# Kernel tuning notes

Measured on AMD Instinct MI355X. Metric: run time of the kernel, lower is better.

The kernel has to match this reference:

```python
import jax, jax.numpy as jnp
import numpy as np

DIM = 64
N_ITER = 2
NUM_USR = 50000
NUM_ENT = 200000
NUM_REL = 32
N_NEIGHBOR = 16
BATCH = 4096


def setup_inputs() -> dict:
    key = jax.random.key(0)
    ks = jax.random.split(key, 12)
    u = jax.random.randint(ks[0], (BATCH,), 0, NUM_USR)
    v = jax.random.randint(ks[1], (BATCH,), 0, NUM_ENT)
    adj = jax.random.randint(ks[2], (NUM_ENT, N_NEIGHBOR), 0, NUM_ENT)
    rel_adj = jax.random.randint(ks[3], (NUM_ENT, N_NEIGHBOR), 0, NUM_REL + 1)
    usr_emb = jax.random.normal(ks[4], (NUM_USR, DIM), dtype=jnp.float32)
    ent_emb = jax.random.normal(ks[5], (NUM_ENT, DIM), dtype=jnp.float32)
    rel_emb = jax.random.normal(ks[6], (NUM_REL + 1, DIM), dtype=jnp.float32)
    # per-hop aggregator Linear(dim, dim) weights (applied as x @ W + b)
    scale = 1.0 / np.sqrt(DIM)
    W0 = jax.random.uniform(ks[7], (DIM, DIM), jnp.float32, -scale, scale)
    b0 = jax.random.uniform(ks[8], (DIM,), jnp.float32, -scale, scale)
    W1 = jax.random.uniform(ks[9], (DIM, DIM), jnp.float32, -scale, scale)
    b1 = jax.random.uniform(ks[10], (DIM,), jnp.float32, -scale, scale)
    return {"u": u, "v": v, "adj": adj, "rel_adj": rel_adj,
            "usr_emb": usr_emb, "ent_emb": ent_emb, "rel_emb": rel_emb,
            "W0": W0, "b0": b0, "W1": W1, "b1": b1}


def reference(u, v, adj, rel_adj, usr_emb, ent_emb, rel_emb, W0, b0, W1, b1):
    B = u.shape[0]
    user = usr_emb[u]  # [B, D]

    # multi-hop neighbor index expansion
    entities = [v[:, None]]            # hop h: [B, n^h]
    relations = []
    for h in range(N_ITER):
        ne = adj[entities[h]].reshape(B, -1)      # [B, n^(h+1)]
        nr = rel_adj[entities[h]].reshape(B, -1)
        entities.append(ne)
        relations.append(nr)

    ent_vecs = [ent_emb[e] for e in entities]     # [B, n^h, D]
    rel_vecs = [rel_emb[r] for r in relations]

    Ws, bs = [W0, W1], [b0, b1]
    for i in range(N_ITER):
        act = jnp.tanh if i == N_ITER - 1 else jax.nn.sigmoid
        nxt = []
        for hop in range(N_ITER - i):
            sv = ent_vecs[hop]                                        # [B, m, D]
            nv = ent_vecs[hop + 1].reshape(B, -1, N_NEIGHBOR, DIM)    # [B, m, n, D]
            nr = rel_vecs[hop].reshape(B, -1, N_NEIGHBOR, DIM)        # [B, m, n, D]
            # user-relation attention over neighbors
            scores = jnp.einsum('bd,bmnd->bmn', user, nr)
            attn = jax.nn.softmax(scores, axis=-1)
            agg = jnp.einsum('bmn,bmnd->bmd', attn, nv)
            out = act((sv + agg) @ Ws[i] + bs[i])
            nxt.append(out)
        ent_vecs = nxt

    item = ent_vecs[0].reshape(B, DIM)
    return jax.nn.sigmoid(jnp.sum(user * item, axis=1))
```

## Files before the change

kernel.cpp:

```cpp
#include <hip/hip_runtime.h>
#include <hip/hip_fp16.h>

#define DIMN 64
#define NNB 16
#define NREL 33
#define WPB 4
#define XSTR 68
#define WFRAG_BYTES 16384

typedef float        floatx4 __attribute__((ext_vector_type(4)));
typedef short        shortx8 __attribute__((ext_vector_type(8)));
typedef unsigned int uintx2  __attribute__((ext_vector_type(2)));

__device__ __forceinline__ float bcastf(float x, int lane) {
    return __int_as_float(__builtin_amdgcn_readlane(__float_as_int(x), lane));
}

__global__ void prep_kernel(const float* __restrict__ W0, unsigned short* __restrict__ wsp,
                            const float* __restrict__ ent, __half* __restrict__ ent16,
                            long n4)
{
    const long tid = (long)blockIdx.x * blockDim.x + threadIdx.x;
    if (tid < 512) {
        const int l = (int)tid & 63;
        const int t = ((int)tid >> 6) & 3;
        const int ks = (int)tid >> 8;
        const int k0 = ks * 32 + (l >> 4) * 8;
        const int n  = t * 16 + (l & 15);
        const unsigned base = ((unsigned)(ks * 4 + t) * 64 + l) * 8;
        #pragma unroll
        for (int j = 0; j < 8; ++j) {
            const float x = W0[(k0 + j) * DIMN + n];
            const unsigned u  = __float_as_uint(x);
            const unsigned uh = u & 0xFFFF0000u;
            const float lf = x - __uint_as_float(uh);
            wsp[base + j]        = (unsigned short)(u >> 16);
            wsp[4096 + base + j] = (unsigned short)(__float_as_uint(lf) >> 16);
        }
    }
    if (ent16) {
        const long stride = (long)gridDim.x * blockDim.x;
        for (long i = tid; i < n4; i += stride) {
            const float4 x = ((const float4*)ent)[i];
            __half2 a = __floats2half2_rn(x.x, x.y);
            __half2 b = __floats2half2_rn(x.z, x.w);
            ((__half2*)ent16)[2 * i]     = a;
            ((__half2*)ent16)[2 * i + 1] = b;
        }
    }
}

__device__ __forceinline__ floatx4 cvt4(uintx2 raw) {
    union { unsigned int u; __half2 h; } a, b;
    a.u = raw.x; b.u = raw.y;
    const float2 f01 = __half22float2(a.h);
    const float2 f23 = __half22float2(b.h);
    return (floatx4){f01.x, f01.y, f23.x, f23.y};
}

template<bool F16>
__global__ __launch_bounds__(64 * WPB, 4)
void kgs_kernel(const int* __restrict__ u, const int* __restrict__ v,
                const int* __restrict__ adj, const int* __restrict__ rel_adj,
                const float* __restrict__ usr_emb, const float* __restrict__ ent_emb,
                const __half* __restrict__ ent16,
                const float* __restrict__ rel_emb,
                const float* __restrict__ W0, const float* __restrict__ b0,
                const float* __restrict__ W1, const float* __restrict__ b1,
                const unsigned short* __restrict__ wsp,
                float* __restrict__ out, int B)
{
    const int tid  = threadIdx.x;
    const int wid  = tid >> 6;
    const int d    = tid & 63;
    const int n16  = d & 15;
    const int quad = d >> 4;
    int b = blockIdx.x * WPB + wid;
    if (b >= B) b = B - 1;

    __shared__ __align__(16) float user_sh[WPB][DIMN];
    __shared__ float ur_sh[WPB][NREL + 3];
    __shared__ __align__(16) float sv_sh[WPB][NNB * XSTR];
    __shared__ __align__(16) float gbuf[WPB][NNB * XSTR];

    const int uu = u[b];
    const int vv = v[b];

    const float user_d = usr_emb[(size_t)uu * DIMN + d];
    const int e1n = adj[vv * NNB + n16];
    const int r1n = rel_adj[vv * NNB + n16];
    float sv0;
    if constexpr (F16) sv0 = __half2float(ent16[(size_t)vv * DIMN + d]);
    else               sv0 = ent_emb[(size_t)vv * DIMN + d];
    user_sh[wid][d] = user_d;

    floatx4 svv[4];
    #pragma unroll
    for (int q = 0; q < 4; ++q) {
        const int em = __shfl(e1n, 4 * q + quad);
        if constexpr (F16)
            svv[q] = cvt4(*(const uintx2*)(ent16 + (size_t)em * DIMN + 4 * n16));
        else
            svv[q] = *(const floatx4*)(ent_emb + (size_t)em * DIMN + 4 * n16);
    }

    int e2n_r[NNB], r2n_r[NNB];
    #pragma unroll
    for (int m = 0; m < NNB; ++m) {
        const int em = __builtin_amdgcn_readlane(e1n, m);
        e2n_r[m] = adj[em * NNB + n16];
        r2n_r[m] = rel_adj[em * NNB + n16];
    }

    if (d < NREL) {
        const float* re = rel_emb + d * DIMN;
        float acc = 0.f;
        #pragma unroll
        for (int k = 0; k < DIMN; k += 4) {
            const float4 uk = *(const float4*)(&user_sh[wid][k]);
            const float4 rk = *(const float4*)(re + k);
            acc = fmaf(uk.x, rk.x, acc);
            acc = fmaf(uk.y, rk.y, acc);
            acc = fmaf(uk.z, rk.z, acc);
            acc = fmaf(uk.w, rk.w, acc);
        }
        ur_sh[wid][d] = acc;
    }

    #pragma unroll
    for (int q = 0; q < 4; ++q)
        *(floatx4*)(&sv_sh[wid][(4 * q + quad) * XSTR + 4 * n16]) = svv[q];

    float attn[NNB];
    #pragma unroll
    for (int m = 0; m < NNB; ++m) {
        const float e = __expf(ur_sh[wid][r2n_r[m]]);
        float s = e;
        s += __shfl_xor(s, 1);
        s += __shfl_xor(s, 2);
        s += __shfl_xor(s, 4);
        s += __shfl_xor(s, 8);
        attn[m] = e * __builtin_amdgcn_rcpf(s);
    }

    #pragma unroll
    for (int m = 0; m < NNB; ++m) {
        floatx4 acc4 = (floatx4){0.f, 0.f, 0.f, 0.f};
        #pragma unroll
        for (int q = 0; q < 4; ++q) {
            const int src = 4 * q + quad;
            const int en  = __shfl(e2n_r[m], src);
            floatx4 g;
            if constexpr (F16)
                g = cvt4(*(const uintx2*)(ent16 + (size_t)en * DIMN + 4 * n16));
            else
                g = *(const floatx4*)(ent_emb + (size_t)en * DIMN + 4 * n16);
            const float aw = __shfl(attn[m], src);
            acc4[0] = fmaf(aw, g[0], acc4[0]);
            acc4[1] = fmaf(aw, g[1], acc4[1]);
            acc4[2] = fmaf(aw, g[2], acc4[2]);
            acc4[3] = fmaf(aw, g[3], acc4[3]);
        }
        #pragma unroll
        for (int c = 0; c < 4; ++c) {
            acc4[c] += __shfl_xor(acc4[c], 16);
            acc4[c] += __shfl_xor(acc4[c], 32);
        }
        if (d < 16)
            *(floatx4*)(&gbuf[wid][m * XSTR + 4 * d]) = acc4;
    }

    shortx8 Ahi[2], Alo[2];
    #pragma unroll
    for (int ks = 0; ks < 2; ++ks) {
        const int off = (d & 15) * XSTR + quad * 8 + ks * 32;
        const floatx4 sa = *(const floatx4*)(&sv_sh[wid][off]);
        const floatx4 sb = *(const floatx4*)(&sv_sh[wid][off + 4]);
        const floatx4 ga = *(const floatx4*)(&gbuf[wid][off]);
        const floatx4 gb = *(const floatx4*)(&gbuf[wid][off + 4]);
        unsigned uh[8], ul[8];
        #pragma unroll
        for (int j = 0; j < 8; ++j) {
            const float x = (j < 4) ? (sa[j] + ga[j]) : (sb[j - 4] + gb[j - 4]);
            const unsigned ub = __float_as_uint(x);
            uh[j] = ub & 0xFFFF0000u;
            ul[j] = __float_as_uint(x - __uint_as_float(uh[j]));
        }
        union { int i[4]; shortx8 s; } ch, cl;
        #pragma unroll
        for (int p = 0; p < 4; ++p) {
            ch.i[p] = (int)(uh[2 * p + 1] | (uh[2 * p] >> 16));
            cl.i[p] = (int)((ul[2 * p + 1] & 0xFFFF0000u) | (ul[2 * p] >> 16));
        }
        Ahi[ks] = ch.s;
        Alo[ks] = cl.s;
    }

    const shortx8* wf = (const shortx8*)wsp;
    floatx4 acc[4];
    #pragma unroll
    for (int t = 0; t < 4; ++t) acc[t] = (floatx4){0.f, 0.f, 0.f, 0.f};
    #pragma unroll
    for (int t = 0; t < 4; ++t) {
        #pragma unroll
        for (int ks = 0; ks < 2; ++ks) {
            const int f = ks * 4 + t;
            const shortx8 bhi = wf[f * 64 + d];
            const shortx8 blo = wf[512 + f * 64 + d];
            acc[t] = __builtin_amdgcn_mfma_f32_16x16x32_bf16(Ahi[ks], bhi, acc[t], 0, 0, 0);
            acc[t] = __builtin_amdgcn_mfma_f32_16x16x32_bf16(Ahi[ks], blo, acc[t], 0, 0, 0);
            acc[t] = __builtin_amdgcn_mfma_f32_16x16x32_bf16(Alo[ks], bhi, acc[t], 0, 0, 0);
        }
    }

    #pragma unroll
    for (int t = 0; t < 4; ++t) {
        const float bv = b0[t * 16 + n16];
        #pragma unroll
        for (int reg = 0; reg < 4; ++reg) {
            const float o = acc[t][reg] + bv;
            const int m = quad * 4 + reg;
            gbuf[wid][m * XSTR + t * 16 + n16] = 1.f / (1.f + __expf(-o));
        }
    }

    const float e0 = __expf(ur_sh[wid][r1n]);
    float sum0 = e0;
    sum0 += __shfl_xor(sum0, 1);
    sum0 += __shfl_xor(sum0, 2);
    sum0 += __shfl_xor(sum0, 4);
    sum0 += __shfl_xor(sum0, 8);
    const float attn0 = e0 * __builtin_amdgcn_rcpf(sum0);

    float agg0 = 0.f, agg1 = 0.f;
    #pragma unroll
    for (int n = 0; n < NNB; ++n) {
        const float an = bcastf(attn0, n);
        agg0 = fmaf(an, sv_sh[wid][n * XSTR + d], agg0);
        agg1 = fmaf(an, gbuf[wid][n * XSTR + d], agg1);
    }

    const float x0 = sv0 + agg0;
    float a0 = 0.f, a1 = 0.f, a2 = 0.f, a3 = 0.f;
    for (int k = 0; k < DIMN; k += 4) {
        const float* wr = W0 + k * DIMN;
        a0 = fmaf(bcastf(x0, k + 0), wr[d], a0);
        a1 = fmaf(bcastf(x0, k + 1), wr[DIMN + d], a1);
        a2 = fmaf(bcastf(x0, k + 2), wr[2 * DIMN + d], a2);
        a3 = fmaf(bcastf(x0, k + 3), wr[3 * DIMN + d], a3);
    }
    const float o0 = b0[d] + ((a0 + a1) + (a2 + a3));
    const float h0 = 1.f / (1.f + __expf(-o0));

    const float x1 = h0 + agg1;
    float c0 = 0.f, c1 = 0.f, c2 = 0.f, c3 = 0.f;
    for (int k = 0; k < DIMN; k += 4) {
        const float* wr = W1 + k * DIMN;
        c0 = fmaf(bcastf(x1, k + 0), wr[d], c0);
        c1 = fmaf(bcastf(x1, k + 1), wr[DIMN + d], c1);
        c2 = fmaf(bcastf(x1, k + 2), wr[2 * DIMN + d], c2);
        c3 = fmaf(bcastf(x1, k + 3), wr[3 * DIMN + d], c3);
    }
    const float o1 = b1[d] + ((c0 + c1) + (c2 + c3));
    const float item_d = 1.f - 2.f / (1.f + __expf(2.f * o1));

    float p = user_d * item_d;
    p += __shfl_xor(p, 1);
    p += __shfl_xor(p, 2);
    p += __shfl_xor(p, 4);
    p += __shfl_xor(p, 8);
    p += __shfl_xor(p, 16);
    p += __shfl_xor(p, 32);
    if (d == 0) out[b] = 1.f / (1.f + __expf(-p));
}

extern "C" void kernel_launch(void* const* d_in, const int* in_sizes, int n_in,
                              void* d_out, int out_size, void* d_ws, size_t ws_size,
                              hipStream_t stream) {
    const int*   u       = (const int*)d_in[0];
    const int*   v       = (const int*)d_in[1];
    const int*   adj     = (const int*)d_in[2];
    const int*   rel_adj = (const int*)d_in[3];
    const float* usr_emb = (const float*)d_in[4];
    const float* ent_emb = (const float*)d_in[5];
    const float* rel_emb = (const float*)d_in[6];
    const float* W0      = (const float*)d_in[7];
    const float* b0      = (const float*)d_in[8];
    const float* W1      = (const float*)d_in[9];
    const float* b1      = (const float*)d_in[10];
    float* out = (float*)d_out;
    unsigned short* wsp = (unsigned short*)d_ws;

    const int B = in_sizes[0];
    const long nent = (long)in_sizes[5];
    const size_t need = (size_t)WFRAG_BYTES + (size_t)nent * sizeof(__half);
    const bool use16 = (ws_size >= need) && ((nent & 3) == 0);
    __half* ent16 = use16 ? (__half*)((char*)d_ws + WFRAG_BYTES) : nullptr;

    const long n4 = nent / 4;
    const int conv_blocks = use16 ? 6400 : 2;
    prep_kernel<<<dim3(conv_blocks), dim3(256), 0, stream>>>(W0, wsp, ent_emb, ent16, n4);

    const int grid = (B + WPB - 1) / WPB;
    if (use16)
        kgs_kernel<true><<<dim3(grid), dim3(64 * WPB), 0, stream>>>(
            u, v, adj, rel_adj, usr_emb, ent_emb, ent16, rel_emb, W0, b0, W1, b1,
            wsp, out, B);
    else
        kgs_kernel<false><<<dim3(grid), dim3(64 * WPB), 0, stream>>>(
            u, v, adj, rel_adj, usr_emb, ent_emb, nullptr, rel_emb, W0, b0, W1, b1,
            wsp, out, B);
}
```

Before: 156.4 us.

## Split each batch element across two wavefronts with block-level sync

Each batch element is now handled by two wavefronts instead of one. Each wave gathers half of the hop-2 neighbours, and the hop-1 MFMA linear and the hop-0 scalar linear run concurrently on different waves. Work is coordinated through shared memory and __syncthreads, and the launch-bounds occupancy hint is raised to 8 blocks. The conversion kernel also packs its fp16 stores into one 64-bit write. The goal is to shorten per-element latency and raise parallelism for the latency-bound gathers, at the cost of block barriers and idle waves in the final stage.

```diff
diff --git a/kernel.cpp b/kernel.cpp
--- a/kernel.cpp
+++ b/kernel.cpp
@@ -4,7 +4,7 @@
 #define DIMN 64
 #define NNB 16
 #define NREL 33
-#define WPB 4
+#define EPB 2
 #define XSTR 68
 #define WFRAG_BYTES 16384
 
@@ -42,10 +42,10 @@
         const long stride = (long)gridDim.x * blockDim.x;
         for (long i = tid; i < n4; i += stride) {
             const float4 x = ((const float4*)ent)[i];
-            __half2 a = __floats2half2_rn(x.x, x.y);
-            __half2 b = __floats2half2_rn(x.z, x.w);
-            ((__half2*)ent16)[2 * i]     = a;
-            ((__half2*)ent16)[2 * i + 1] = b;
+            union { __half2 h[2]; uintx2 u; } pk;
+            pk.h[0] = __floats2half2_rn(x.x, x.y);
+            pk.h[1] = __floats2half2_rn(x.z, x.w);
+            ((uintx2*)ent16)[i] = pk.u;
         }
     }
 }
@@ -59,7 +59,7 @@
 }
 
 template<bool F16>
-__global__ __launch_bounds__(64 * WPB, 4)
+__global__ __launch_bounds__(64 * 4, 8)
 void kgs_kernel(const int* __restrict__ u, const int* __restrict__ v,
                 const int* __restrict__ adj, const int* __restrict__ rel_adj,
                 const float* __restrict__ usr_emb, const float* __restrict__ ent_emb,
@@ -75,13 +75,15 @@
     const int d    = tid & 63;
     const int n16  = d & 15;
     const int quad = d >> 4;
-    int b = blockIdx.x * WPB + wid;
+    const int e    = wid >> 1;
+    const int half = wid & 1;
+    int b = blockIdx.x * EPB + e;
     if (b >= B) b = B - 1;
 
-    __shared__ __align__(16) float user_sh[WPB][DIMN];
-    __shared__ float ur_sh[WPB][NREL + 3];
-    __shared__ __align__(16) float sv_sh[WPB][NNB * XSTR];
-    __shared__ __align__(16) float gbuf[WPB][NNB * XSTR];
+    __shared__ __align__(16) float user_sh[EPB][DIMN];
+    __shared__ float ur_sh[EPB][NREL + 3];
+    __shared__ __align__(16) float sv_sh[EPB][NNB * XSTR];
+    __shared__ __align__(16) float gbuf[EPB][NNB * XSTR];
 
     const int uu = u[b];
     const int vv = v[b];
@@ -92,70 +94,75 @@
     float sv0;
     if constexpr (F16) sv0 = __half2float(ent16[(size_t)vv * DIMN + d]);
     else               sv0 = ent_emb[(size_t)vv * DIMN + d];
-    user_sh[wid][d] = user_d;
-
-    floatx4 svv[4];
+    user_sh[e][d] = user_d;
+
     #pragma unroll
-    for (int q = 0; q < 4; ++q) {
+    for (int qq = 0; qq < 2; ++qq) {
+        const int q  = 2 * half + qq;
         const int em = __shfl(e1n, 4 * q + quad);
+        floatx4 sq;
         if constexpr (F16)
-            svv[q] = cvt4(*(const uintx2*)(ent16 + (size_t)em * DIMN + 4 * n16));
+            sq = cvt4(*(const uintx2*)(ent16 + (size_t)em * DIMN + 4 * n16));
         else
-            svv[q] = *(const floatx4*)(ent_emb + (size_t)em * DIMN + 4 * n16);
-    }
-
-    int e2n_r[NNB], r2n_r[NNB];
+            sq = *(const floatx4*)(ent_emb + (size_t)em * DIMN + 4 * n16);
+        *(floatx4*)(&sv_sh[e][(4 * q + quad) * XSTR + 4 * n16]) = sq;
+    }
+
+    int e2n_r[8], r2n_r[8];
     #pragma unroll
-    for (int m = 0; m < NNB; ++m) {
-        const int em = __builtin_amdgcn_readlane(e1n, m);
-        e2n_r[m] = adj[em * NNB + n16];
-        r2n_r[m] = rel_adj[em * NNB + n16];
-    }
-
-    if (d < NREL) {
-        const float* re = rel_emb + d * DIMN;
-        float acc = 0.f;
-        #pragma unroll
-        for (int k = 0; k < DIMN; k += 4) {
-            const float4 uk = *(const float4*)(&user_sh[wid][k]);
-            const float4 rk = *(const float4*)(re + k);
-            acc = fmaf(uk.x, rk.x, acc);
-            acc = fmaf(uk.y, rk.y, acc);
-            acc = fmaf(uk.z, rk.z, acc);
-            acc = fmaf(uk.w, rk.w, acc);
-        }
-        ur_sh[wid][d] = acc;
-    }
-
+    for (int j = 0; j < 8; ++j) {
+        const int em = __builtin_amdgcn_readlane(e1n, 8 * half + j);
+        e2n_r[j] = adj[em * NNB + n16];
+        r2n_r[j] = rel_adj[em * NNB + n16];
+    }
+
+    {
+        const int lim = half ? 16 : 17;
+        if (d < lim) {
+            const int rr = half * 17 + d;
+            const float* re = rel_emb + rr * DIMN;
+            float acc = 0.f;
+            #pragma unroll
+            for (int k = 0; k < DIMN; k += 4) {
+                const float4 uk = *(const float4*)(&user_sh[e][k]);
+                const float4 rk = *(const float4*)(re + k);
+                acc = fmaf(uk.x, rk.x, acc);
+                acc = fmaf(uk.y, rk.y, acc);
+                acc = fmaf(uk.z, rk.z, acc);
+                acc = fmaf(uk.w, rk.w, acc);
+            }
+            ur_sh[e][rr] = acc;
+        }
+    }
+
+    __syncthreads();
+
+    float attn[8];
     #pragma unroll
-    for (int q = 0; q < 4; ++q)
-        *(floatx4*)(&sv_sh[wid][(4 * q + quad) * XSTR + 4 * n16]) = svv[q];
-
-    float attn[NNB];
-    #pragma unroll
-    for (int m = 0; m < NNB; ++m) {
-        const float e = __expf(ur_sh[wid][r2n_r[m]]);
-        float s = e;
+    for (int j = 0; j < 8; ++j) {
+        const float ex = __expf(ur_sh[e][r2n_r[j]]);
+        float s = ex;
         s += __shfl_xor(s, 1);
         s += __shfl_xor(s, 2);
         s += __shfl_xor(s, 4);
         s += __shfl_xor(s, 8);
-        attn[m] = e * __builtin_amdgcn_rcpf(s);
+        attn[j] = ex * __builtin_amdgcn_rcpf(s);
     }
 
     #pragma unroll
-    for (int m = 0; m < NNB; ++m) {
+    for (int j = 0; j < 8; ++j) {
+        const int m = 8 * half + j;
         floatx4 acc4 = (floatx4){0.f, 0.f, 0.f, 0.f};
         #pragma unroll
         for (int q = 0; q < 4; ++q) {
             const int src = 4 * q + quad;
-            const int en  = __shfl(e2n_r[m], src);
+            const int en  = __shfl(e2n_r[j], src);
             floatx4 g;
             if constexpr (F16)
                 g = cvt4(*(const uintx2*)(ent16 + (size_t)en * DIMN + 4 * n16));
             else
                 g = *(const floatx4*)(ent_emb + (size_t)en * DIMN + 4 * n16);
-            const float aw = __shfl(attn[m], src);
+            const float aw = __shfl(attn[j], src);
             acc4[0] = fmaf(aw, g[0], acc4[0]);
             acc4[1] = fmaf(aw, g[1], acc4[1]);
             acc4[2] = fmaf(aw, g[2], acc4[2]);
@@ -167,111 +174,122 @@
             acc4[c] += __shfl_xor(acc4[c], 32);
         }
         if (d < 16)
-            *(floatx4*)(&gbuf[wid][m * XSTR + 4 * d]) = acc4;
-    }
-
-    shortx8 Ahi[2], Alo[2];
-    #pragma unroll
-    for (int ks = 0; ks < 2; ++ks) {
-        const int off = (d & 15) * XSTR + quad * 8 + ks * 32;
-        const floatx4 sa = *(const floatx4*)(&sv_sh[wid][off]);
-        const floatx4 sb = *(const floatx4*)(&sv_sh[wid][off + 4]);
-        const floatx4 ga = *(const floatx4*)(&gbuf[wid][off]);
-        const floatx4 gb = *(const floatx4*)(&gbuf[wid][off + 4]);
-        unsigned uh[8], ul[8];
-        #pragma unroll
-        for (int j = 0; j < 8; ++j) {
-            const float x = (j < 4) ? (sa[j] + ga[j]) : (sb[j - 4] + gb[j - 4]);
-            const unsigned ub = __float_as_uint(x);
-            uh[j] = ub & 0xFFFF0000u;
-            ul[j] = __float_as_uint(x - __uint_as_float(uh[j]));
-        }
-        union { int i[4]; shortx8 s; } ch, cl;
-        #pragma unroll
-        for (int p = 0; p < 4; ++p) {
-            ch.i[p] = (int)(uh[2 * p + 1] | (uh[2 * p] >> 16));
-            cl.i[p] = (int)((ul[2 * p + 1] & 0xFFFF0000u) | (ul[2 * p] >> 16));
-        }
-        Ahi[ks] = ch.s;
-        Alo[ks] = cl.s;
-    }
-
-    const shortx8* wf = (const shortx8*)wsp;
-    floatx4 acc[4];
-    #pragma unroll
-    for (int t = 0; t < 4; ++t) acc[t] = (floatx4){0.f, 0.f, 0.f, 0.f};
-    #pragma unroll
-    for (int t = 0; t < 4; ++t) {
+            *(floatx4*)(&gbuf[e][m * XSTR + 4 * d]) = acc4;
+    }
+
+    __syncthreads();
+
+    float attn0 = 0.f, h0 = 0.f;
+    if (half == 1) {
+        shortx8 Ahi[2], Alo[2];
         #pragma unroll
         for (int ks = 0; ks < 2; ++ks) {
-            const int f = ks * 4 + t;
-            const shortx8 bhi = wf[f * 64 + d];
-            const shortx8 blo = wf[512 + f * 64 + d];
-            acc[t] = __builtin_amdgcn_mfma_f32_16x16x32_bf16(Ahi[ks], bhi, acc[t], 0, 0, 0);
-            acc[t] = __builtin_amdgcn_mfma_f32_16x16x32_bf16(Ahi[ks], blo, acc[t], 0, 0, 0);
-            acc[t] = __builtin_amdgcn_mfma_f32_16x16x32_bf16(Alo[ks], bhi, acc[t], 0, 0, 0);
-        }
-    }
-
-    #pragma unroll
-    for (int t = 0; t < 4; ++t) {
-        const float bv = b0[t * 16 + n16];
-        #pragma unroll
-        for (int reg = 0; reg < 4; ++reg) {
-            const float o = acc[t][reg] + bv;
-            const int m = quad * 4 + reg;
-            gbuf[wid][m * XSTR + t * 16 + n16] = 1.f / (1.f + __expf(-o));
-        }
-    }
-
-    const float e0 = __expf(ur_sh[wid][r1n]);
-    float sum0 = e0;
-    sum0 += __shfl_xor(sum0, 1);
-    sum0 += __shfl_xor(sum0, 2);
-    sum0 += __shfl_xor(sum0, 4);
-    sum0 += __shfl_xor(sum0, 8);
-    const float attn0 = e0 * __builtin_amdgcn_rcpf(sum0);
-
-    float agg0 = 0.f, agg1 = 0.f;
-    #pragma unroll
-    for (int n = 0; n < NNB; ++n) {
-        const float an = bcastf(attn0, n);
-        agg0 = fmaf(an, sv_sh[wid][n * XSTR + d], agg0);
-        agg1 = fmaf(an, gbuf[wid][n * XSTR + d], agg1);
-    }
-
-    const float x0 = sv0 + agg0;
-    float a0 = 0.f, a1 = 0.f, a2 = 0.f, a3 = 0.f;
-    for (int k = 0; k < DIMN; k += 4) {
-        const float* wr = W0 + k * DIMN;
-        a0 = fmaf(bcastf(x0, k + 0), wr[d], a0);
-        a1 = fmaf(bcastf(x0, k + 1), wr[DIMN + d], a1);
-        a2 = fmaf(bcastf(x0, k + 2), wr[2 * DIMN + d], a2);
-        a3 = fmaf(bcastf(x0, k + 3), wr[3 * DIMN + d], a3);
-    }
-    const float o0 = b0[d] + ((a0 + a1) + (a2 + a3));
-    const float h0 = 1.f / (1.f + __expf(-o0));
-
-    const float x1 = h0 + agg1;
-    float c0 = 0.f, c1 = 0.f, c2 = 0.f, c3 = 0.f;
-    for (int k = 0; k < DIMN; k += 4) {
-        const float* wr = W1 + k * DIMN;
-        c0 = fmaf(bcastf(x1, k + 0), wr[d], c0);
-        c1 = fmaf(bcastf(x1, k + 1), wr[DIMN + d], c1);
-        c2 = fmaf(bcastf(x1, k + 2), wr[2 * DIMN + d], c2);
-        c3 = fmaf(bcastf(x1, k + 3), wr[3 * DIMN + d], c3);
-    }
-    const float o1 = b1[d] + ((c0 + c1) + (c2 + c3));
-    const float item_d = 1.f - 2.f / (1.f + __expf(2.f * o1));
-
-    float p = user_d * item_d;
-    p += __shfl_xor(p, 1);
-    p += __shfl_xor(p, 2);
-    p += __shfl_xor(p, 4);
-    p += __shfl_xor(p, 8);
-    p += __shfl_xor(p, 16);
-    p += __shfl_xor(p, 32);
-    if (d == 0) out[b] = 1.f / (1.f + __expf(-p));
+            const int off = n16 * XSTR + quad * 8 + ks * 32;
+            const floatx4 sa = *(const floatx4*)(&sv_sh[e][off]);
+            const floatx4 sb = *(const floatx4*)(&sv_sh[e][off + 4]);
+            const floatx4 ga = *(const floatx4*)(&gbuf[e][off]);
+            const floatx4 gb = *(const floatx4*)(&gbuf[e][off + 4]);
+            unsigned uh[8], ul[8];
+            #pragma unroll
+            for (int j = 0; j < 8; ++j) {
+                const float x = (j < 4) ? (sa[j] + ga[j]) : (sb[j - 4] + gb[j - 4]);
+                const unsigned ub = __float_as_uint(x);
+                uh[j] = ub & 0xFFFF0000u;
+                ul[j] = __float_as_uint(x - __uint_as_float(uh[j]));
+            }
+            union { int i[4]; shortx8 s; } ch, cl;
+            #pragma unroll
+            for (int p = 0; p < 4; ++p) {
+                ch.i[p] = (int)(uh[2 * p + 1] | (uh[2 * p] >> 16));
+                cl.i[p] = (int)((ul[2 * p + 1] & 0xFFFF0000u) | (ul[2 * p] >> 16));
+            }
+            Ahi[ks] = ch.s;
+            Alo[ks] = cl.s;
+        }
+
+        const shortx8* wf = (const shortx8*)wsp;
+        floatx4 acc[4];
+        #pragma unroll
+        for (int t = 0; t < 4; ++t) acc[t] = (floatx4){0.f, 0.f, 0.f, 0.f};
+        #pragma unroll
+        for (int t = 0; t < 4; ++t) {
+            #pragma unroll
+            for (int ks = 0; ks < 2; ++ks) {
+                const int f = ks * 4 + t;
+                const shortx8 bhi = wf[f * 64 + d];
+                const shortx8 blo = wf[512 + f * 64 + d];
+                acc[t] = __builtin_amdgcn_mfma_f32_16x16x32_bf16(Ahi[ks], bhi, acc[t], 0, 0, 0);
+                acc[t] = __builtin_amdgcn_mfma_f32_16x16x32_bf16(Ahi[ks], blo, acc[t], 0, 0, 0);
+                acc[t] = __builtin_amdgcn_mfma_f32_16x16x32_bf16(Alo[ks], bhi, acc[t], 0, 0, 0);
+            }
+        }
+
+        #pragma unroll
+        for (int t = 0; t < 4; ++t) {
+            const float bv = b0[t * 16 + n16];
+            #pragma unroll
+            for (int reg = 0; reg < 4; ++reg) {
+                const float o = acc[t][reg] + bv;
+                const int m = quad * 4 + reg;
+                gbuf[e][m * XSTR + t * 16 + n16] = 1.f / (1.f + __expf(-o));
+            }
+        }
+    } else {
+        const float e0 = __expf(ur_sh[e][r1n]);
+        float sum0 = e0;
+        sum0 += __shfl_xor(sum0, 1);
+        sum0 += __shfl_xor(sum0, 2);
+        sum0 += __shfl_xor(sum0, 4);
+        sum0 += __shfl_xor(sum0, 8);
+        attn0 = e0 * __builtin_amdgcn_rcpf(sum0);
+
+        float agg0 = 0.f;
+        #pragma unroll
+        for (int n = 0; n < NNB; ++n)
+            agg0 = fmaf(bcastf(attn0, n), sv_sh[e][n * XSTR + d], agg0);
+
+        const float x0 = sv0 + agg0;
+        float a0 = 0.f, a1 = 0.f, a2 = 0.f, a3 = 0.f;
+        for (int k = 0; k < DIMN; k += 4) {
+            const float* wr = W0 + k * DIMN;
+            a0 = fmaf(bcastf(x0, k + 0), wr[d], a0);
+            a1 = fmaf(bcastf(x0, k + 1), wr[DIMN + d], a1);
+            a2 = fmaf(bcastf(x0, k + 2), wr[2 * DIMN + d], a2);
+            a3 = fmaf(bcastf(x0, k + 3), wr[3 * DIMN + d], a3);
+        }
+        const float o0 = b0[d] + ((a0 + a1) + (a2 + a3));
+        h0 = 1.f / (1.f + __expf(-o0));
+    }
+
+    __syncthreads();
+
+    if (half == 0) {
+        float agg1 = 0.f;
+        #pragma unroll
+        for (int n = 0; n < NNB; ++n)
+            agg1 = fmaf(bcastf(attn0, n), gbuf[e][n * XSTR + d], agg1);
+
+        const float x1 = h0 + agg1;
+        float c0 = 0.f, c1 = 0.f, c2 = 0.f, c3 = 0.f;
+        for (int k = 0; k < DIMN; k += 4) {
+            const float* wr = W1 + k * DIMN;
+            c0 = fmaf(bcastf(x1, k + 0), wr[d], c0);
+            c1 = fmaf(bcastf(x1, k + 1), wr[DIMN + d], c1);
+            c2 = fmaf(bcastf(x1, k + 2), wr[2 * DIMN + d], c2);
+            c3 = fmaf(bcastf(x1, k + 3), wr[3 * DIMN + d], c3);
+        }
+        const float o1 = b1[d] + ((c0 + c1) + (c2 + c3));
+        const float item_d = 1.f - 2.f / (1.f + __expf(2.f * o1));
+
+        float p = user_d * item_d;
+        p += __shfl_xor(p, 1);
+        p += __shfl_xor(p, 2);
+        p += __shfl_xor(p, 4);
+        p += __shfl_xor(p, 8);
+        p += __shfl_xor(p, 16);
+        p += __shfl_xor(p, 32);
+        if (d == 0) out[b] = 1.f / (1.f + __expf(-p));
+    }
 }
 
 extern "C" void kernel_launch(void* const* d_in, const int* in_sizes, int n_in,
@@ -301,13 +319,13 @@
     const int conv_blocks = use16 ? 6400 : 2;
     prep_kernel<<<dim3(conv_blocks), dim3(256), 0, stream>>>(W0, wsp, ent_emb, ent16, n4);
 
-    const int grid = (B + WPB - 1) / WPB;
+    const int grid = (B + EPB - 1) / EPB;
     if (use16)
-        kgs_kernel<true><<<dim3(grid), dim3(64 * WPB), 0, stream>>>(
+        kgs_kernel<true><<<dim3(grid), dim3(256), 0, stream>>>(
             u, v, adj, rel_adj, usr_emb, ent_emb, ent16, rel_emb, W0, b0, W1, b1,
             wsp, out, B);
     else
-        kgs_kernel<false><<<dim3(grid), dim3(64 * WPB), 0, stream>>>(
+        kgs_kernel<false><<<dim3(grid), dim3(256), 0, stream>>>(
             u, v, adj, rel_adj, usr_emb, ent_emb, nullptr, rel_emb, W0, b0, W1, b1,
             wsp, out, B);
 }
```

Result: slower. 182.8 us (+16.9%).
